# Performance work log

Measured on AMD Instinct MI355X. Metric: run time of the kernel, lower is better.

Reference implementation:

```python
import jax, jax.numpy as jnp
import numpy as np
import math

T, B, E, H = 1024, 4, 512, 8
HD = E // H

def setup_inputs() -> dict:
    key = jax.random.key(0)
    ks = jax.random.split(key, 6)
    return {
        "query": jax.random.normal(ks[0], (T, B, E), dtype=jnp.float32),
        "dist": jax.random.normal(ks[1], (B, T, T, H), dtype=jnp.float32) * 0.1,
        "in_proj_weight": jax.random.normal(ks[2], (3 * E, E), dtype=jnp.float32) * 0.02,
        "in_proj_bias": jax.random.normal(ks[3], (3 * E,), dtype=jnp.float32) * 0.02,
        "out_proj_weight": jax.random.normal(ks[4], (E, E), dtype=jnp.float32) * 0.02,
        "out_proj_bias": jax.random.normal(ks[5], (E,), dtype=jnp.float32) * 0.02,
    }

def reference(query, dist, in_proj_weight, in_proj_bias, out_proj_weight, out_proj_bias):
    t, b, e = query.shape
    # packed in-projection (self-attention: q=k=v=query)
    qkv = query @ in_proj_weight.T + in_proj_bias          # [T,B,3E]
    q, k, v = jnp.split(qkv, 3, axis=-1)                   # each [T,B,E]
    def heads(x):
        return x.reshape(t, b * H, HD).transpose(1, 0, 2)  # [B*H,T,HD]
    q, k, v = heads(q), heads(k), heads(v)
    q = q / math.sqrt(HD)
    attn = jnp.einsum('bte,bse->bts', q, k)                # [B*H,T,T]
    # distance/structure bias: [B,T,T,H] -> [B,H,T,T] -> [B*H,T,T]
    bias = jnp.transpose(dist, (0, 3, 1, 2)).reshape(b * H, t, t)
    attn = jax.nn.softmax(attn + bias, axis=-1)
    out = jnp.einsum('bts,bse->bte', attn, v)              # [B*H,T,HD]
    out = out.transpose(1, 0, 2).reshape(t, b, e)          # [T,B,E]
    out = out @ out_proj_weight.T + out_proj_bias
    return out
```

## Files before the change

### kernel.cpp

```cpp
#include <hip/hip_runtime.h>
#include <math.h>

typedef __bf16 bf16;
typedef bf16 bf16x8 __attribute__((ext_vector_type(8)));
typedef bf16 bf16x4 __attribute__((ext_vector_type(4)));
typedef float f32x4 __attribute__((ext_vector_type(4)));

#define T_DIM 1024
#define B_DIM 4
#define E_DIM 512
#define H_DIM 8
#define HD_DIM 64
#define BH_DIM 32

__device__ __forceinline__ f32x4 mfma16(bf16x8 a, bf16x8 b, f32x4 c) {
    return __builtin_amdgcn_mfma_f32_16x16x32_bf16(a, b, c, 0, 0, 0);
}

__device__ __forceinline__ bf16x4 cvt4(f32x4 v) {
    bf16x4 o;
    o[0] = (bf16)v[0]; o[1] = (bf16)v[1]; o[2] = (bf16)v[2]; o[3] = (bf16)v[3];
    return o;
}

#define CVT_Q_V   524288
#define CVT_W1_V  196608
__global__ __launch_bounds__(256)
void prep(const float* __restrict__ dist, bf16* __restrict__ bias_t,
          const float* __restrict__ q, const float* __restrict__ w1,
          const float* __restrict__ w2, bf16* __restrict__ qo,
          bf16* __restrict__ w1o, bf16* __restrict__ w2o) {
    __shared__ __align__(16) bf16 tile[8 * 1032];
    if (blockIdx.x >= 4096) {
        long v = (long)(blockIdx.x - 4096) * 256 + threadIdx.x;
        const float* src; bf16* dst;
        if (v < CVT_Q_V)                { src = q;  dst = qo; }
        else if (v < CVT_Q_V + CVT_W1_V){ v -= CVT_Q_V;  src = w1; dst = w1o; }
        else                            { v -= CVT_Q_V + CVT_W1_V; src = w2; dst = w2o; }
        f32x4 f = *(const f32x4*)(src + v * 4);
        *(bf16x4*)(dst + v * 4) = cvt4(f);
        return;
    }
    const int bt = blockIdx.x;
    const int b = bt >> 10, t = bt & 1023;
    const int tid = threadIdx.x;
    const float* src = dist + ((long)bt << 13) + tid * 32;
    const int s0 = tid * 4;
    float v[32];
#pragma unroll
    for (int j = 0; j < 8; j++) {
        f32x4 f = *(const f32x4*)(src + j * 4);
        v[j * 4 + 0] = f[0]; v[j * 4 + 1] = f[1];
        v[j * 4 + 2] = f[2]; v[j * 4 + 3] = f[3];
    }
#pragma unroll
    for (int h = 0; h < 8; h++)
#pragma unroll
        for (int si = 0; si < 4; si++)
            tile[h * 1032 + s0 + si] = (bf16)v[si * 8 + h];
    __syncthreads();
#pragma unroll
    for (int rep = 0; rep < 4; rep++) {
        int slot = rep * 256 + tid;
        int h = slot >> 7;
        int sc = (slot & 127) * 8;
        bf16x8 o = *(const bf16x8*)&tile[h * 1032 + sc];
        *(bf16x8*)&bias_t[((long)(b * 8 + h) * T_DIM + t) * T_DIM + sc] = o;
    }
}

template<int TM, int TN, int MODE>
__global__ __launch_bounds__(256)
void gemm_t(const bf16* __restrict__ A, const bf16* __restrict__ Bt,
            const float* __restrict__ bias, int K, int N,
            float* __restrict__ out, bf16* __restrict__ qb,
            bf16* __restrict__ kb, bf16* __restrict__ vb) {
    constexpr int FM = TM / 32, FN = TN / 32;
    constexpr int PA = TM / 64, PB = TN / 64;
    __shared__ __align__(16) bf16 As[2][TM * 72];
    __shared__ __align__(16) bf16 Bs[2][TN * 72];
    const int tid  = threadIdx.x;
    const int lane = tid & 63;
    const int wave = tid >> 6;
    const int quad = lane >> 4;
    const int l15  = lane & 15;
    const int wm = wave & 1, wn = wave >> 1;
    const int m0 = blockIdx.x * TM, n0 = blockIdx.y * TN;

    f32x4 acc[FM][FN] = {};

    const int sr = tid >> 2;
    const int sc = (tid & 3) * 16;

    bf16x8 ra[PA][2], rb[PB][2];
#pragma unroll
    for (int p = 0; p < PA; p++) {
        const bf16* src = &A[(long)(m0 + p * 64 + sr) * K + sc];
        ra[p][0] = *(const bf16x8*)(src);
        ra[p][1] = *(const bf16x8*)(src + 8);
    }
#pragma unroll
    for (int p = 0; p < PB; p++) {
        const bf16* src = &Bt[(long)(n0 + p * 64 + sr) * K + sc];
        rb[p][0] = *(const bf16x8*)(src);
        rb[p][1] = *(const bf16x8*)(src + 8);
    }

    const int NK = K >> 6;
    for (int i = 0; i < NK; i++) {
        const int cur = i & 1;
        bf16* as = As[cur];
        bf16* bs = Bs[cur];
#pragma unroll
        for (int p = 0; p < PA; p++) {
            *(bf16x8*)&as[(p * 64 + sr) * 72 + sc]     = ra[p][0];
            *(bf16x8*)&as[(p * 64 + sr) * 72 + sc + 8] = ra[p][1];
        }
#pragma unroll
        for (int p = 0; p < PB; p++) {
            *(bf16x8*)&bs[(p * 64 + sr) * 72 + sc]     = rb[p][0];
            *(bf16x8*)&bs[(p * 64 + sr) * 72 + sc + 8] = rb[p][1];
        }
        __syncthreads();

        if (i + 1 < NK) {
            const int kn = (i + 1) << 6;
#pragma unroll
            for (int p = 0; p < PA; p++) {
                const bf16* src = &A[(long)(m0 + p * 64 + sr) * K + kn + sc];
                ra[p][0] = *(const bf16x8*)(src);
                ra[p][1] = *(const bf16x8*)(src + 8);
            }
#pragma unroll
            for (int p = 0; p < PB; p++) {
                const bf16* src = &Bt[(long)(n0 + p * 64 + sr) * K + kn + sc];
                rb[p][0] = *(const bf16x8*)(src);
                rb[p][1] = *(const bf16x8*)(src + 8);
            }
        }

#pragma unroll
        for (int kk = 0; kk < 64; kk += 32) {
            bf16x8 af[FM], bfr[FN];
#pragma unroll
            for (int mb = 0; mb < FM; mb++)
                af[mb] = *(const bf16x8*)&as[(wm * (TM / 2) + mb * 16 + l15) * 72 + kk + quad * 8];
#pragma unroll
            for (int nb = 0; nb < FN; nb++)
                bfr[nb] = *(const bf16x8*)&bs[(wn * (TN / 2) + nb * 16 + l15) * 72 + kk + quad * 8];
#pragma unroll
            for (int mb = 0; mb < FM; mb++)
#pragma unroll
                for (int nb = 0; nb < FN; nb++)
                    acc[mb][nb] = mfma16(af[mb], bfr[nb], acc[mb][nb]);
        }
    }

#pragma unroll
    for (int mb = 0; mb < FM; mb++) {
#pragma unroll
        for (int nb = 0; nb < FN; nb++) {
            int n = n0 + wn * (TN / 2) + nb * 16 + l15;
            float bv = bias[n];
#pragma unroll
            for (int r = 0; r < 4; r++) {
                int m = m0 + wm * (TM / 2) + mb * 16 + quad * 4 + r;
                float v = acc[mb][nb][r] + bv;
                if (MODE == 0) {
                    out[(long)m * N + n] = v;
                } else {
                    int t = m >> 2, b = m & 3;
                    int sec = n >> 9, j = n & 511;
                    int h = j >> 6, hd = j & 63;
                    int bh = b * 8 + h;
                    if (sec == 0)
                        qb[((long)bh * T_DIM + t) * HD_DIM + hd] = (bf16)(v * 0.125f);
                    else if (sec == 1)
                        kb[((long)bh * T_DIM + t) * HD_DIM + hd] = (bf16)v;
                    else
                        vb[((long)bh * HD_DIM + hd) * T_DIM + t] = (bf16)v;
                }
            }
        }
    }
}

__global__ __launch_bounds__(256)
void attn_kernel(const bf16* __restrict__ qb, const bf16* __restrict__ kb,
                 const bf16* __restrict__ vb, const bf16* __restrict__ bias_t,
                 bf16* __restrict__ ctxb) {
    __shared__ __align__(16) bf16 Ks[64 * 72];
    __shared__ __align__(16) bf16 Vts[64 * 72];
    __shared__ __align__(16) bf16 Ps[4 * 16 * 72];
    const int tid  = threadIdx.x;
    const int lane = tid & 63;
    const int wave = tid >> 6;
    const int quad = lane >> 4;
    const int l15  = lane & 15;
    const int bid  = blockIdx.x;
    const int bh   = bid >> 4;
    const int qt   = bid & 15;
    const int b    = bh >> 3, h = bh & 7;
    const int qrow = qt * 64 + wave * 16 + l15;

    bf16x8 qa0 = *(const bf16x8*)&qb[((long)bh * T_DIM + qrow) * HD_DIM + quad * 8];
    bf16x8 qa1 = *(const bf16x8*)&qb[((long)bh * T_DIM + qrow) * HD_DIM + 32 + quad * 8];

    f32x4 oacc[4] = {};
    float lsum[4] = {0.f, 0.f, 0.f, 0.f};

    const int r0 = tid >> 3;
    const int c0 = (tid & 7) * 8;

    const bf16* dp = bias_t + ((long)bh * T_DIM + qt * 64 + wave * 16 + quad * 4) * T_DIM;

    bf16x8 pk0, pk1, pv0, pv1;
    float pbias[16];
    pk0 = *(const bf16x8*)&kb[((long)bh * T_DIM + r0) * HD_DIM + c0];
    pk1 = *(const bf16x8*)&kb[((long)bh * T_DIM + r0 + 32) * HD_DIM + c0];
    pv0 = *(const bf16x8*)&vb[((long)bh * HD_DIM + r0) * T_DIM + c0];
    pv1 = *(const bf16x8*)&vb[((long)bh * HD_DIM + r0 + 32) * T_DIM + c0];
#pragma unroll
    for (int r = 0; r < 4; r++)
#pragma unroll
        for (int nb = 0; nb < 4; nb++)
            pbias[r * 4 + nb] = (float)dp[(long)r * T_DIM + nb * 16 + l15];

    for (int st = 0; st < T_DIM; st += 64) {
        __syncthreads();
        *(bf16x8*)&Ks[r0 * 72 + c0]         = pk0;
        *(bf16x8*)&Ks[(r0 + 32) * 72 + c0]  = pk1;
        *(bf16x8*)&Vts[r0 * 72 + c0]        = pv0;
        *(bf16x8*)&Vts[(r0 + 32) * 72 + c0] = pv1;
        __syncthreads();

        if (st + 64 < T_DIM) {
            const int sn = st + 64;
            pk0 = *(const bf16x8*)&kb[((long)bh * T_DIM + sn + r0) * HD_DIM + c0];
            pk1 = *(const bf16x8*)&kb[((long)bh * T_DIM + sn + r0 + 32) * HD_DIM + c0];
            pv0 = *(const bf16x8*)&vb[((long)bh * HD_DIM + r0) * T_DIM + sn + c0];
            pv1 = *(const bf16x8*)&vb[((long)bh * HD_DIM + r0 + 32) * T_DIM + sn + c0];
        }

        f32x4 sacc[4] = {};
        __builtin_amdgcn_s_setprio(1);
#pragma unroll
        for (int kk = 0; kk < 64; kk += 32) {
            bf16x8 a = (kk == 0) ? qa0 : qa1;
#pragma unroll
            for (int nb = 0; nb < 4; nb++) {
                bf16x8 bfr = *(const bf16x8*)&Ks[(nb * 16 + l15) * 72 + kk + quad * 8];
                sacc[nb] = mfma16(a, bfr, sacc[nb]);
            }
        }
        __builtin_amdgcn_s_setprio(0);

        bf16* pw = &Ps[wave * 16 * 72];
#pragma unroll
        for (int r = 0; r < 4; r++) {
            float rs = 0.f;
#pragma unroll
            for (int nb = 0; nb < 4; nb++) {
                float p = __expf(sacc[nb][r] + pbias[r * 4 + nb]);
                rs += p;
                pw[(quad * 4 + r) * 72 + nb * 16 + l15] = (bf16)p;
            }
            lsum[r] += rs;
        }

        if (st + 64 < T_DIM) {
            const int sn = st + 64;
#pragma unroll
            for (int r = 0; r < 4; r++)
#pragma unroll
                for (int nb = 0; nb < 4; nb++)
                    pbias[r * 4 + nb] = (float)dp[(long)r * T_DIM + sn + nb * 16 + l15];
        }

        __builtin_amdgcn_s_setprio(1);
#pragma unroll
        for (int kk = 0; kk < 64; kk += 32) {
            bf16x8 ap = *(const bf16x8*)&pw[l15 * 72 + kk + quad * 8];
#pragma unroll
            for (int nb = 0; nb < 4; nb++) {
                bf16x8 bv2 = *(const bf16x8*)&Vts[(nb * 16 + l15) * 72 + kk + quad * 8];
                oacc[nb] = mfma16(ap, bv2, oacc[nb]);
            }
        }
        __builtin_amdgcn_s_setprio(0);
    }

#pragma unroll
    for (int r = 0; r < 4; r++) {
#pragma unroll
        for (int msk = 1; msk < 16; msk <<= 1)
            lsum[r] += __shfl_xor(lsum[r], msk);
    }

#pragma unroll
    for (int nb = 0; nb < 4; nb++) {
#pragma unroll
        for (int r = 0; r < 4; r++) {
            int t  = qt * 64 + wave * 16 + quad * 4 + r;
            int hd = nb * 16 + l15;
            float o = oacc[nb][r] / lsum[r];
            ctxb[((long)t * B_DIM + b) * E_DIM + h * HD_DIM + hd] = (bf16)o;
        }
    }
}

extern "C" void kernel_launch(void* const* d_in, const int* in_sizes, int n_in,
                              void* d_out, int out_size, void* d_ws, size_t ws_size,
                              hipStream_t stream) {
    const float* query = (const float*)d_in[0];
    const float* dist  = (const float*)d_in[1];
    const float* win   = (const float*)d_in[2];
    const float* bin   = (const float*)d_in[3];
    const float* wout  = (const float*)d_in[4];
    const float* bout  = (const float*)d_in[5];
    float* out = (float*)d_out;

    bf16* bias_t = (bf16*)d_ws;
    bf16* qb   = bias_t + ((long)BH_DIM * T_DIM * T_DIM);
    bf16* kb   = qb + (1 << 21);
    bf16* vb   = kb + (1 << 21);
    bf16* qbf  = vb + (1 << 21);
    bf16* w1bf = qbf + (1 << 21);
    bf16* w2bf = w1bf + 786432;
    bf16* ctxb = w2bf + 262144;

    prep<<<dim3(7168), 256, 0, stream>>>(dist, bias_t, query, win, wout,
                                         qbf, w1bf, w2bf);
    gemm_t<64, 192, 1><<<dim3(64, 8), 256, 0, stream>>>(
        qbf, w1bf, bin, 512, 1536, nullptr, qb, kb, vb);
    attn_kernel<<<dim3(512), 256, 0, stream>>>(qb, kb, vb, bias_t, ctxb);
    gemm_t<64, 64, 0><<<dim3(64, 8), 256, 0, stream>>>(
        ctxb, w2bf, bout, 512, 512, out, nullptr, nullptr, nullptr);
}
```

Measured before the change: 268.1 us.

## Load GEMM tiles directly to LDS with global_load_lds, single-buffered

Replaces the register-staged double-buffered GEMM tile loading with direct global-to-LDS loads (global_load_lds, 16 bytes per lane) into an unpadded single LDS buffer, adding a trailing barrier per k-step. The in-projection tile is also changed from 64x192 to 64x128 with a 12-column grid. This aims to cut register pressure and LDS write instructions, but it drops the prefetch overlap and removes the padding, which risks LDS bank conflicts on the fragment reads. The GEMMs are small next to the attention kernel, so the effect on total time is likely limited.

Result: no change. 271.2 us (+1.2%).

```diff
diff --git a/kernel.cpp b/kernel.cpp
--- a/kernel.cpp
+++ b/kernel.cpp
@@ -1,5 +1,6 @@
 #include <hip/hip_runtime.h>
 #include <math.h>
+#include <stdint.h>
 
 typedef __bf16 bf16;
 typedef bf16 bf16x8 __attribute__((ext_vector_type(8)));
@@ -21,6 +22,13 @@
     bf16x4 o;
     o[0] = (bf16)v[0]; o[1] = (bf16)v[1]; o[2] = (bf16)v[2]; o[3] = (bf16)v[3];
     return o;
+}
+
+__device__ __forceinline__ void gll16(const bf16* g, bf16* l) {
+    __builtin_amdgcn_global_load_lds(
+        (const __attribute__((address_space(1))) uint32_t*)g,
+        (__attribute__((address_space(3))) uint32_t*)l,
+        16, 0, 0);
 }
 
 #define CVT_Q_V   524288
@@ -76,9 +84,10 @@
             float* __restrict__ out, bf16* __restrict__ qb,
             bf16* __restrict__ kb, bf16* __restrict__ vb) {
     constexpr int FM = TM / 32, FN = TN / 32;
-    constexpr int PA = TM / 64, PB = TN / 64;
-    __shared__ __align__(16) bf16 As[2][TM * 72];
-    __shared__ __align__(16) bf16 Bs[2][TN * 72];
+    constexpr int NCA = TM / 8;
+    constexpr int NCB = TN / 8;
+    __shared__ __align__(16) bf16 As[TM * 64];
+    __shared__ __align__(16) bf16 Bs[TN * 64];
     const int tid  = threadIdx.x;
     const int lane = tid & 63;
     const int wave = tid >> 6;
@@ -89,71 +98,32 @@
 
     f32x4 acc[FM][FN] = {};
 
-    const int sr = tid >> 2;
-    const int sc = (tid & 3) * 16;
-
-    bf16x8 ra[PA][2], rb[PB][2];
-#pragma unroll
-    for (int p = 0; p < PA; p++) {
-        const bf16* src = &A[(long)(m0 + p * 64 + sr) * K + sc];
-        ra[p][0] = *(const bf16x8*)(src);
-        ra[p][1] = *(const bf16x8*)(src + 8);
-    }
-#pragma unroll
-    for (int p = 0; p < PB; p++) {
-        const bf16* src = &Bt[(long)(n0 + p * 64 + sr) * K + sc];
-        rb[p][0] = *(const bf16x8*)(src);
-        rb[p][1] = *(const bf16x8*)(src + 8);
-    }
-
-    const int NK = K >> 6;
-    for (int i = 0; i < NK; i++) {
-        const int cur = i & 1;
-        bf16* as = As[cur];
-        bf16* bs = Bs[cur];
-#pragma unroll
-        for (int p = 0; p < PA; p++) {
-            *(bf16x8*)&as[(p * 64 + sr) * 72 + sc]     = ra[p][0];
-            *(bf16x8*)&as[(p * 64 + sr) * 72 + sc + 8] = ra[p][1];
-        }
-#pragma unroll
-        for (int p = 0; p < PB; p++) {
-            *(bf16x8*)&bs[(p * 64 + sr) * 72 + sc]     = rb[p][0];
-            *(bf16x8*)&bs[(p * 64 + sr) * 72 + sc + 8] = rb[p][1];
-        }
+    const int srow = lane >> 3;
+    const int scol = (lane & 7) * 8;
+
+    for (int k0 = 0; k0 < K; k0 += 64) {
+        for (int c = wave; c < NCA; c += 4)
+            gll16(&A[(long)(m0 + c * 8 + srow) * K + k0 + scol], &As[c * 512]);
+        for (int c = wave; c < NCB; c += 4)
+            gll16(&Bt[(long)(n0 + c * 8 + srow) * K + k0 + scol], &Bs[c * 512]);
         __syncthreads();
-
-        if (i + 1 < NK) {
-            const int kn = (i + 1) << 6;
-#pragma unroll
-            for (int p = 0; p < PA; p++) {
-                const bf16* src = &A[(long)(m0 + p * 64 + sr) * K + kn + sc];
-                ra[p][0] = *(const bf16x8*)(src);
-                ra[p][1] = *(const bf16x8*)(src + 8);
-            }
-#pragma unroll
-            for (int p = 0; p < PB; p++) {
-                const bf16* src = &Bt[(long)(n0 + p * 64 + sr) * K + kn + sc];
-                rb[p][0] = *(const bf16x8*)(src);
-                rb[p][1] = *(const bf16x8*)(src + 8);
-            }
-        }
 
 #pragma unroll
         for (int kk = 0; kk < 64; kk += 32) {
             bf16x8 af[FM], bfr[FN];
 #pragma unroll
             for (int mb = 0; mb < FM; mb++)
-                af[mb] = *(const bf16x8*)&as[(wm * (TM / 2) + mb * 16 + l15) * 72 + kk + quad * 8];
+                af[mb] = *(const bf16x8*)&As[(wm * (TM / 2) + mb * 16 + l15) * 64 + kk + quad * 8];
 #pragma unroll
             for (int nb = 0; nb < FN; nb++)
-                bfr[nb] = *(const bf16x8*)&bs[(wn * (TN / 2) + nb * 16 + l15) * 72 + kk + quad * 8];
+                bfr[nb] = *(const bf16x8*)&Bs[(wn * (TN / 2) + nb * 16 + l15) * 64 + kk + quad * 8];
 #pragma unroll
             for (int mb = 0; mb < FM; mb++)
 #pragma unroll
                 for (int nb = 0; nb < FN; nb++)
                     acc[mb][nb] = mfma16(af[mb], bfr[nb], acc[mb][nb]);
         }
+        __syncthreads();
     }
 
 #pragma unroll
@@ -331,7 +301,7 @@
 
     prep<<<dim3(7168), 256, 0, stream>>>(dist, bias_t, query, win, wout,
                                          qbf, w1bf, w2bf);
-    gemm_t<64, 192, 1><<<dim3(64, 8), 256, 0, stream>>>(
+    gemm_t<64, 128, 1><<<dim3(64, 12), 256, 0, stream>>>(
         qbf, w1bf, bin, 512, 1536, nullptr, qb, kb, vb);
     attn_kernel<<<dim3(512), 256, 0, stream>>>(qb, kb, vb, bias_t, ctxb);
     gemm_t<64, 64, 0><<<dim3(64, 8), 256, 0, stream>>>(
```
